# Performance work log

Measured on AMD Instinct MI355X. Metric: run time of the kernel, lower is better.

## Reference

```python
import jax, jax.numpy as jnp
import numpy as np
from jax import lax

B, T, D_IN = 16, 512, 128
H_ENC, D_LAT, H_CTX, H_PRED = 512, 256, 512, 512
K_STEPS, TEMP = 12, 0.1


def setup_inputs() -> dict:
    ks = jax.random.split(jax.random.key(0), 8)
    def w(i, fi, fo):
        return jax.random.normal(ks[i], (fi, fo), jnp.float32) * (1.0 / float(np.sqrt(fi)))
    return {
        "x": jax.random.normal(ks[0], (B, T, D_IN), jnp.float32),
        "enc_w1": w(1, D_IN, H_ENC), "enc_b1": jnp.zeros((H_ENC,), jnp.float32),
        "enc_w2": w(2, H_ENC, H_ENC), "enc_b2": jnp.zeros((H_ENC,), jnp.float32),
        "enc_w3": w(3, H_ENC, D_LAT), "enc_b3": jnp.zeros((D_LAT,), jnp.float32),
        "gru_wi": w(4, D_LAT, 3 * H_CTX), "gru_bi": jnp.zeros((3 * H_CTX,), jnp.float32),
        "gru_wh": w(5, H_CTX, 3 * H_CTX), "gru_bhn": jnp.zeros((H_CTX,), jnp.float32),
        "pred_w1": w(6, H_CTX, H_PRED), "pred_b1": jnp.zeros((H_PRED,), jnp.float32),
        "pred_w2": w(7, H_PRED, D_LAT), "pred_b2": jnp.zeros((D_LAT,), jnp.float32),
    }


def _gru(z, gru_wi, gru_bi, gru_wh, gru_bhn):
    # flax GRUCell: r=sig(Wir x + bir + Whr h); u=sig(Wiz x + biz + Whz h);
    Bsz = z.shape[0]
    H = gru_wh.shape[0]
    xi = z @ gru_wi + gru_bi          # [B, T, 3H] precomputed input projections
    xi = jnp.swapaxes(xi, 0, 1)       # [T, B, 3H]

    def step(h, x_t):
        hp = h @ gru_wh               # [B, 3H]
        xr, xu, xn = jnp.split(x_t, 3, axis=-1)
        hr, hu, hn = jnp.split(hp, 3, axis=-1)
        r = jax.nn.sigmoid(xr + hr)
        u = jax.nn.sigmoid(xu + hu)
        n = jnp.tanh(xn + r * (hn + gru_bhn))
        h_new = (1.0 - u) * n + u * h
        return h_new, h_new

    h0 = jnp.zeros((Bsz, H), z.dtype)
    _, outs = lax.scan(step, h0, xi)  # [T, B, H]
    return jnp.swapaxes(outs, 0, 1)   # [B, T, H]


def reference(x, enc_w1, enc_b1, enc_w2, enc_b2, enc_w3, enc_b3,
              gru_wi, gru_bi, gru_wh, gru_bhn,
              pred_w1, pred_b1, pred_w2, pred_b2):
    # Encoder MLP
    h = jax.nn.relu(x @ enc_w1 + enc_b1)
    h = jax.nn.relu(h @ enc_w2 + enc_b2)
    z = h @ enc_w3 + enc_b3                         # [B, T, D_LAT]
    # GRU context network
    c = _gru(z, gru_wi, gru_bi, gru_wh, gru_bhn)    # [B, T, H_CTX]
    # InfoNCE loss (prediction net is identical across k, so hoist it)
    c_t = c[:, :-K_STEPS, :].reshape(-1, c.shape[-1])   # [N, H_CTX], N=B*(T-K)
    p = jax.nn.relu(c_t @ pred_w1 + pred_b1) @ pred_w2 + pred_b2
    p = p / jnp.linalg.norm(p, axis=1, keepdims=True)   # [N, D_LAT]
    total = jnp.zeros((), z.dtype)
    for k in range(1, K_STEPS + 1):
        zt = z[:, k:T - K_STEPS + k, :].reshape(-1, z.shape[-1])
        zt = zt / jnp.linalg.norm(zt, axis=1, keepdims=True)
        sim = (p @ zt.T) / TEMP                         # [N, N]
        # -mean(diag(log_softmax)) = -mean(diag(sim) - logsumexp(sim, axis=1))
        total = total + (-jnp.mean(jnp.diagonal(sim) - jax.nn.logsumexp(sim, axis=1)))
    loss = total / K_STEPS
    return z, c, loss
```

## Files before the change

kernel.cpp:

```cpp
#include <hip/hip_runtime.h>
#include <cstdint>
#include <cstddef>

typedef unsigned short u16;
typedef unsigned int   u32;
typedef unsigned long long u64;
typedef __attribute__((ext_vector_type(8))) short bf16x8;
typedef __attribute__((ext_vector_type(4))) float f32x4;
typedef __attribute__((ext_vector_type(4))) unsigned int u32x4;

typedef __attribute__((address_space(1))) const unsigned int as1c_uint;
typedef __attribute__((address_space(3))) unsigned int as3_uint;

__device__ __forceinline__ void async16(const void* g, void* l) {
  __builtin_amdgcn_global_load_lds((as1c_uint*)g, (as3_uint*)l, 16, 0, 0);
}
__device__ __forceinline__ float bf2f(u16 u) {
  return __uint_as_float(((u32)u) << 16);
}
__device__ __forceinline__ u16 f2bf(float x) {
  u32 u = __float_as_uint(x);
  u32 r = u + 0x7FFFu + ((u >> 16) & 1u);
  return (u16)(r >> 16);
}

__device__ __forceinline__ u32 ld_u32_ic(const void* p) {
  u32 v;
  asm volatile("global_load_dword %0, %1, off sc0 sc1\n\ts_waitcnt vmcnt(0)"
               : "=v"(v) : "v"(p) : "memory");
  return v;
}
__device__ __forceinline__ void st_u32_ic(void* p, u32 v) {
  asm volatile("global_store_dword %0, %1, off sc0 sc1" :: "v"(p), "v"(v) : "memory");
}
__device__ __forceinline__ void ld_h64_ic(const void* p, u32x4& a, u32x4& b,
                                          u32x4& c, u32x4& d) {
  asm volatile(
      "global_load_dwordx4 %0, %4, off sc0 sc1\n\t"
      "global_load_dwordx4 %1, %4, off offset:16 sc0 sc1\n\t"
      "global_load_dwordx4 %2, %4, off offset:32 sc0 sc1\n\t"
      "global_load_dwordx4 %3, %4, off offset:48 sc0 sc1\n\t"
      "s_waitcnt vmcnt(0)"
      : "=&v"(a), "=&v"(b), "=&v"(c), "=&v"(d) : "v"(p) : "memory");
}

__global__ void cvt_k(const float4* __restrict__ in, ushort4* __restrict__ out) {
  int i = blockIdx.x * 256 + threadIdx.x;
  float4 v = in[i];
  ushort4 o;
  o.x = f2bf(v.x); o.y = f2bf(v.y); o.z = f2bf(v.z); o.w = f2bf(v.w);
  out[i] = o;
}

__global__ void tr_k(const float* __restrict__ in, u16* __restrict__ out, int K, int N) {
  __shared__ u16 t[32][33];
  int bn = blockIdx.x * 32, bk = blockIdx.y * 32;
  int x = threadIdx.x, y = threadIdx.y;
#pragma unroll
  for (int i = 0; i < 32; i += 8)
    t[y + i][x] = f2bf(in[(size_t)(bk + y + i) * N + bn + x]);
  __syncthreads();
#pragma unroll
  for (int i = 0; i < 32; i += 8)
    out[(size_t)(bn + y + i) * K + bk + x] = t[x][y + i];
}

__global__ __launch_bounds__(256) void gemm_k(
    const u16* __restrict__ A, const u16* __restrict__ Bt,
    const float* __restrict__ bias, u16* __restrict__ Cbf, float* __restrict__ Cf,
    int N, int K, int act) {
  __shared__ __align__(16) u16 As[128 * 32];
  __shared__ __align__(16) u16 Bs[128 * 32];
  int tid = threadIdx.x;
  int lane = tid & 63, w = tid >> 6;
  int wm = w >> 1, wn = w & 1;
  int mm = lane & 15, kh = lane >> 4;
  int m0 = blockIdx.y * 128, n0 = blockIdx.x * 128;

  f32x4 zero = {0.f, 0.f, 0.f, 0.f};
  f32x4 acc[4][4];
#pragma unroll
  for (int i = 0; i < 4; ++i)
#pragma unroll
    for (int j = 0; j < 4; ++j) acc[i][j] = zero;

  for (int kt = 0; kt < K; kt += 32) {
#pragma unroll
    for (int it = 0; it < 2; ++it) {
      int q = tid + it * 256;
      int row = q >> 2, kc = (q & 3) * 8;
      async16(A  + (size_t)(m0 + row) * K + kt + kc, &As[q * 8]);
      async16(Bt + (size_t)(n0 + row) * K + kt + kc, &Bs[q * 8]);
    }
    __syncthreads();
    bf16x8 av[4], bv[4];
#pragma unroll
    for (int i = 0; i < 4; ++i) {
      av[i] = *(const bf16x8*)&As[(wm * 64 + i * 16 + mm) * 32 + kh * 8];
      bv[i] = *(const bf16x8*)&Bs[(wn * 64 + i * 16 + mm) * 32 + kh * 8];
    }
#pragma unroll
    for (int im = 0; im < 4; ++im)
#pragma unroll
      for (int in = 0; in < 4; ++in)
        acc[im][in] = __builtin_amdgcn_mfma_f32_16x16x32_bf16(av[im], bv[in], acc[im][in], 0, 0, 0);
    __syncthreads();
  }

#pragma unroll
  for (int im = 0; im < 4; ++im)
#pragma unroll
    for (int in = 0; in < 4; ++in)
#pragma unroll
      for (int r = 0; r < 4; ++r) {
        int gm = m0 + wm * 64 + im * 16 + kh * 4 + r;
        int gn = n0 + wn * 64 + in * 16 + mm;
        float v = acc[im][in][r] + bias[gn];
        if (act) v = fmaxf(v, 0.f);
        size_t off = (size_t)gm * N + gn;
        if (Cbf) Cbf[off] = f2bf(v);
        if (Cf)  Cf[off]  = v;
      }
}

__global__ __launch_bounds__(256) void norm_k(const u16* __restrict__ in,
                                              u16* __restrict__ out, int pack) {
  int row = blockIdx.x * 4 + (threadIdx.x >> 6);
  int lane = threadIdx.x & 63;
  ushort4 v = ((const ushort4*)(in + (size_t)row * 256))[lane];
  float a = bf2f(v.x), b = bf2f(v.y), c = bf2f(v.z), d = bf2f(v.w);
  float s = a * a + b * b + c * c + d * d;
#pragma unroll
  for (int o = 32; o; o >>= 1) s += __shfl_xor(s, o);
  float rn = rsqrtf(s);
  int orow = row;
  if (pack) {
    int bb = row >> 9, tt = row & 511;
    if (tt >= 500) return;
    orow = bb * 500 + tt;
  }
  ushort4 o4;
  o4.x = f2bf(a * rn); o4.y = f2bf(b * rn);
  o4.z = f2bf(c * rn); o4.w = f2bf(d * rn);
  *(ushort4*)(out + (size_t)orow * 256 + lane * 4) = o4;
}

#define HS 520

__global__ __launch_bounds__(512, 1) void gru_k(
    const u16* __restrict__ xi, const float* __restrict__ WH,
    const float* __restrict__ BHN, float* __restrict__ cf,
    u16* __restrict__ cbf, u16* hbuf, u32* flags) {
  __shared__ __align__(16) u16 hs[16 * HS];
  __shared__ float xis[2 * 1536];
  __shared__ float gts[1536];
  __shared__ float hnf[512];

  int tid = threadIdx.x;
  int role = blockIdx.x;
  int c0 = role * 32;

  int lane = tid & 63, w = tid >> 6;
  int mm = lane & 15, kh = lane >> 4;

  bf16x8 wf[16];
  if (w < 6) {
    int gcol = (w >> 1) * 512 + c0 + (w & 1) * 16 + mm;
    int kb = kh * 8;
#pragma unroll
    for (int kk = 0; kk < 16; ++kk) {
      bf16x8 tf;
#pragma unroll
      for (int j = 0; j < 8; ++j)
        tf[j] = (short)f2bf(WH[(size_t)(kk * 32 + kb + j) * 1536 + gcol]);
      wf[kk] = tf;
    }
  }
  int cr = tid >> 4, cj = (tid & 15) * 2;
  float bhn0 = 0.f, bhn1 = 0.f;
  if (w < 4) { bhn0 = BHN[c0 + cj]; bhn1 = BHN[c0 + cj + 1]; }

  int tt = tid - 384;
  size_t xoff[12];
  u16 xpre[12];
  if (w >= 6) {
#pragma unroll
    for (int j = 0; j < 12; ++j) {
      int v = j * 128 + tt;
      int b = v / 96, q = v - b * 96;
      int gcol = (q >> 5) * 512 + c0 + (q & 31);
      xoff[j] = (size_t)b * 512 * 1536 + gcol;
      xis[v] = bf2f(xi[xoff[j]]);
    }
#pragma unroll
    for (int j = 0; j < 12; ++j) xpre[j] = xi[xoff[j] + 1536];
  }

  for (int t = 0; t < 512; ++t) {
    if (w < 4) {
      if (t == 0) {
        for (int i = tid; i < 16 * HS; i += 256) hs[i] = 0;
      } else {
        int iter = 0;
        const u32* fl = &flags[tid & 15];
        while (ld_u32_ic(fl) < (u32)t) { if (++iter > (1 << 22)) break; }
        const u16* hb = hbuf + (size_t)(t & 1) * 8192 + (tid >> 4) * 512 + (tid & 15) * 32;
        u32x4 a, b, c, d;
        ld_h64_ic(hb, a, b, c, d);
        u32x4* dst = (u32x4*)&hs[(tid >> 4) * HS + (tid & 15) * 32];
        dst[0] = a; dst[1] = b; dst[2] = c; dst[3] = d;
      }
    } else if (w >= 6) {
      if (t > 0) {
        int v = tt * 4;
        int b = v >> 5, col = v & 31;
        size_t co = ((size_t)b * 512 + (t - 1)) * 512 + c0 + col;
        float4 o;
        o.x = hnf[v]; o.y = hnf[v + 1]; o.z = hnf[v + 2]; o.w = hnf[v + 3];
        *(float4*)&cf[co] = o;
        uint2 pk;
        pk.x = (u32)f2bf(o.x) | ((u32)f2bf(o.y) << 16);
        pk.y = (u32)f2bf(o.z) | ((u32)f2bf(o.w) << 16);
        *(uint2*)&cbf[co] = pk;
      }
      if (t < 511) {
        float* xd = &xis[((t + 1) & 1) * 1536];
#pragma unroll
        for (int j = 0; j < 12; ++j) xd[j * 128 + tt] = bf2f(xpre[j]);
      }
      if (t < 510) {
        const u16* xs = xi + (size_t)(t + 2) * 1536;
#pragma unroll
        for (int j = 0; j < 12; ++j) xpre[j] = xs[xoff[j]];
      }
    }
    __syncthreads();

    if (w < 6) {
      f32x4 acc = {0.f, 0.f, 0.f, 0.f};
#pragma unroll
      for (int kk = 0; kk < 16; ++kk) {
        bf16x8 a = *(const bf16x8*)&hs[mm * HS + kk * 32 + kh * 8];
        acc = __builtin_amdgcn_mfma_f32_16x16x32_bf16(a, wf[kk], acc, 0, 0, 0);
      }
      int gc = (w >> 1) * 32 + (w & 1) * 16 + mm;
#pragma unroll
      for (int r = 0; r < 4; ++r) gts[(kh * 4 + r) * 96 + gc] = acc[r];
    }
    __syncthreads();

    if (w < 4) {
      const float* xc = &xis[(t & 1) * 1536] + cr * 96;
      const float* gr_ = &gts[cr * 96];
      float hp0 = bf2f(hs[cr * HS + c0 + cj]);
      float hp1 = bf2f(hs[cr * HS + c0 + cj + 1]);
      float r0 = 1.f / (1.f + __expf(-(xc[cj] + gr_[cj])));
      float u0 = 1.f / (1.f + __expf(-(xc[32 + cj] + gr_[32 + cj])));
      float nx0 = xc[64 + cj] + r0 * (gr_[64 + cj] + bhn0);
      float n0 = 1.f - 2.f / (__expf(2.f * nx0) + 1.f);
      float h0 = (1.f - u0) * n0 + u0 * hp0;
      float r1 = 1.f / (1.f + __expf(-(xc[cj + 1] + gr_[cj + 1])));
      float u1 = 1.f / (1.f + __expf(-(xc[33 + cj] + gr_[33 + cj])));
      float nx1 = xc[65 + cj] + r1 * (gr_[65 + cj] + bhn1);
      float n1 = 1.f - 2.f / (__expf(2.f * nx1) + 1.f);
      float h1v = (1.f - u1) * n1 + u1 * hp1;
      hnf[cr * 32 + cj] = h0;
      hnf[cr * 32 + cj + 1] = h1v;
      u32 pk = (u32)f2bf(h0) | ((u32)f2bf(h1v) << 16);
      st_u32_ic(hbuf + (size_t)((t + 1) & 1) * 8192 + cr * 512 + c0 + cj, pk);
      asm volatile("s_waitcnt vmcnt(0)" ::: "memory");
    }
    __syncthreads();
    if (tid == 0) st_u32_ic(&flags[role], (u32)(t + 1));
  }

  if (w >= 6) {
    int v = tt * 4;
    int b = v >> 5, col = v & 31;
    size_t co = ((size_t)b * 512 + 511) * 512 + c0 + col;
    float4 o;
    o.x = hnf[v]; o.y = hnf[v + 1]; o.z = hnf[v + 2]; o.w = hnf[v + 3];
    *(float4*)&cf[co] = o;
    uint2 pk;
    pk.x = (u32)f2bf(o.x) | ((u32)f2bf(o.y) << 16);
    pk.y = (u32)f2bf(o.z) | ((u32)f2bf(o.w) << 16);
    *(uint2*)&cbf[co] = pk;
  }
}

__global__ __launch_bounds__(256) void sgemm_k(
    const u16* __restrict__ P, const u16* __restrict__ Z,
    float* __restrict__ g, float* __restrict__ diag) {
  __shared__ __align__(16) u16 Ap[128 * 256];
  __shared__ __align__(16) u16 Bs[128 * 32];
  __shared__ float gacc[128 * 128];
  int tid = threadIdx.x;
  int lane = tid & 63, w = tid >> 6;
  int wm = w >> 1, wn = w & 1;
  int mm = lane & 15, kh = lane >> 4;
  int r0 = blockIdx.y * 128, t0 = blockIdx.x * 128;

#pragma unroll
  for (int it = 0; it < 16; ++it) {
    int q = tid + it * 256;
    int row = q >> 5, kc = (q & 31) * 8;
    async16(P + (size_t)(r0 + row) * 256 + kc, &Ap[q * 8]);
  }
  for (int i = tid; i < 128 * 128; i += 256) gacc[i] = 0.f;
  __syncthreads();

  f32x4 zero = {0.f, 0.f, 0.f, 0.f};
  for (int b = 0; b < 16; ++b) {
    int n0 = b * 512 + t0;
    f32x4 acc[4][4];
#pragma unroll
    for (int i = 0; i < 4; ++i)
#pragma unroll
      for (int j = 0; j < 4; ++j) acc[i][j] = zero;

    for (int kk = 0; kk < 8; ++kk) {
#pragma unroll
      for (int it = 0; it < 2; ++it) {
        int q = tid + it * 256;
        int row = q >> 2, kc = (q & 3) * 8;
        async16(Z + (size_t)(n0 + row) * 256 + kk * 32 + kc, &Bs[q * 8]);
      }
      __syncthreads();
      bf16x8 av[4], bv[4];
#pragma unroll
      for (int i = 0; i < 4; ++i) {
        av[i] = *(const bf16x8*)&Ap[(wm * 64 + i * 16 + mm) * 256 + kk * 32 + kh * 8];
        bv[i] = *(const bf16x8*)&Bs[(wn * 64 + i * 16 + mm) * 32 + kh * 8];
      }
#pragma unroll
      for (int im = 0; im < 4; ++im)
#pragma unroll
        for (int in = 0; in < 4; ++in)
          acc[im][in] = __builtin_amdgcn_mfma_f32_16x16x32_bf16(av[im], bv[in], acc[im][in], 0, 0, 0);
      __syncthreads();
    }
#pragma unroll
    for (int im = 0; im < 4; ++im)
#pragma unroll
      for (int in = 0; in < 4; ++in)
#pragma unroll
        for (int r = 0; r < 4; ++r) {
          int row = wm * 64 + im * 16 + kh * 4 + r;
          int col = wn * 64 + in * 16 + mm;
          float s10 = acc[im][in][r] * 10.f;
          gacc[row * 128 + col] += __expf(s10 - 10.f);
          int ig = r0 + row;
          if (ig < 8000) {
            int bi = ig / 500;
            if (bi == b) {
              int ti = ig - bi * 500;
              int dt = t0 + col - ti;
              if (dt >= 1 && dt <= 12) diag[(size_t)ig * 12 + dt - 1] = s10;
            }
          }
        }
  }
  __syncthreads();
  for (int i = tid; i < 128 * 128; i += 256) {
    int row = i >> 7, col = i & 127;
    g[(size_t)(r0 + row) * 512 + t0 + col] = gacc[i];
  }
}

__global__ __launch_bounds__(256) void win_k(const float* __restrict__ g,
                                             const float* __restrict__ diag,
                                             float* __restrict__ acc) {
  __shared__ float lo[4][16], hi[4][16];
  int w = threadIdx.x >> 6, lane = threadIdx.x & 63;
  int row = blockIdx.x * 4 + w;
  const float* gr = g + (size_t)row * 512;
  float4 a = ((const float4*)gr)[lane * 2];
  float4 b = ((const float4*)gr)[lane * 2 + 1];
  float s = a.x + a.y + a.z + a.w + b.x + b.y + b.z + b.w;
#pragma unroll
  for (int o = 32; o; o >>= 1) s += __shfl_xor(s, o);
  if (lane == 0) { lo[w][0]=a.x; lo[w][1]=a.y; lo[w][2]=a.z; lo[w][3]=a.w;
                   lo[w][4]=b.x; lo[w][5]=b.y; lo[w][6]=b.z; lo[w][7]=b.w; }
  if (lane == 1) { lo[w][8]=a.x; lo[w][9]=a.y; lo[w][10]=a.z; lo[w][11]=a.w; }
  if (lane == 62){ hi[w][0]=b.x; hi[w][1]=b.y; hi[w][2]=b.z; hi[w][3]=b.w; }
  if (lane == 63){ hi[w][4]=a.x; hi[w][5]=a.y; hi[w][6]=a.z; hi[w][7]=a.w;
                   hi[w][8]=b.x; hi[w][9]=b.y; hi[w][10]=b.z; hi[w][11]=b.w; }
  __syncthreads();
  float term = 0.f;
  if (lane < 12) {
    int k = lane + 1;
    float pre = 0.f, suf = 0.f;
#pragma unroll
    for (int j = 0; j < 12; ++j) {
      if (j < k) pre += lo[w][j];
      if (j >= k) suf += hi[w][j];
    }
    float W = s - pre - suf;
    term = diag[(size_t)row * 12 + lane] - __logf(W) - 10.f;
  }
#pragma unroll
  for (int o = 32; o; o >>= 1) term += __shfl_xor(term, o);
  if (lane == 0) atomicAdd(acc, term);
}

__global__ void fin_k(const float* acc, float* lout) {
  lout[0] = -acc[0] * (1.f / 96000.f);
}

extern "C" void kernel_launch(void* const* d_in, const int* in_sizes, int n_in,
                              void* d_out, int out_size, void* d_ws, size_t ws_size,
                              hipStream_t stream) {
  (void)in_sizes; (void)n_in; (void)out_size; (void)ws_size;
  const float* x    = (const float*)d_in[0];
  const float* ew1  = (const float*)d_in[1];
  const float* eb1  = (const float*)d_in[2];
  const float* ew2  = (const float*)d_in[3];
  const float* eb2  = (const float*)d_in[4];
  const float* ew3  = (const float*)d_in[5];
  const float* eb3  = (const float*)d_in[6];
  const float* gwi  = (const float*)d_in[7];
  const float* gbi  = (const float*)d_in[8];
  const float* gwh  = (const float*)d_in[9];
  const float* gbhn = (const float*)d_in[10];
  const float* pw1  = (const float*)d_in[11];
  const float* pb1  = (const float*)d_in[12];
  const float* pw2  = (const float*)d_in[13];
  const float* pb2  = (const float*)d_in[14];

  char* W = (char*)d_ws;
  u32*   flags = (u32*)(W + 64);
  float* lacc = (float*)(W + 2048);
  u16*   w1T  = (u16*)(W + 4096);
  u16*   w2T  = (u16*)(W + 135168);
  u16*   w3T  = (u16*)(W + 659456);
  u16*   wiT  = (u16*)(W + 921600);
  u16*   p1T  = (u16*)(W + 1708032);
  u16*   p2T  = (u16*)(W + 2232320);
  u16*   hbuf = (u16*)(W + 2494464);
  float* diag = (float*)(W + 2527232);
  u16*   zhat = (u16*)(W + 2911232);
  u16*   zbf  = (u16*)(W + 7105536);
  u16*   cbf  = (u16*)(W + 7105536);
  u16*   ppk  = (u16*)(W + 7105536);
  u16*   xi   = (u16*)(W + 15494144);
  u16*   xbf  = (u16*)(W + 15494144);
  u16*   h1   = (u16*)(W + 17591296);
  u16*   h2   = (u16*)(W + 25979904);
  float* g    = (float*)(W + 15494144);

  float* zf    = (float*)d_out;
  float* cf    = zf + 2097152;
  float* lout  = zf + 6291456;

  hipMemsetAsync(d_ws, 0, 4096, stream);

  cvt_k<<<1024, 256, 0, stream>>>((const float4*)x, (ushort4*)xbf);

  dim3 tb(32, 8);
  tr_k<<<dim3(16, 4),  tb, 0, stream>>>(ew1, w1T, 128, 512);
  tr_k<<<dim3(16, 16), tb, 0, stream>>>(ew2, w2T, 512, 512);
  tr_k<<<dim3(8, 16),  tb, 0, stream>>>(ew3, w3T, 512, 256);
  tr_k<<<dim3(48, 8),  tb, 0, stream>>>(gwi, wiT, 256, 1536);
  tr_k<<<dim3(16, 16), tb, 0, stream>>>(pw1, p1T, 512, 512);
  tr_k<<<dim3(8, 16),  tb, 0, stream>>>(pw2, p2T, 512, 256);

  gemm_k<<<dim3(4, 64),  256, 0, stream>>>(xbf,  w1T, eb1, h1,  nullptr, 512, 128, 1);
  gemm_k<<<dim3(4, 64),  256, 0, stream>>>(h1,   w2T, eb2, h2,  nullptr, 512, 512, 1);
  gemm_k<<<dim3(2, 64),  256, 0, stream>>>(h2,   w3T, eb3, zbf, zf,      256, 512, 0);
  norm_k<<<2048, 256, 0, stream>>>(zbf, zhat, 0);
  gemm_k<<<dim3(12, 64), 256, 0, stream>>>(zbf,  wiT, gbi, xi,  nullptr, 1536, 256, 0);
  gru_k<<<16, 512, 0, stream>>>(xi, gwh, gbhn, cf, cbf, hbuf, flags);
  gemm_k<<<dim3(4, 64),  256, 0, stream>>>(cbf,  p1T, pb1, h1,  nullptr, 512, 512, 1);
  gemm_k<<<dim3(2, 64),  256, 0, stream>>>(h1,   p2T, pb2, h2,  nullptr, 256, 512, 0);
  norm_k<<<2048, 256, 0, stream>>>(h2, ppk, 1);
  sgemm_k<<<dim3(4, 63), 256, 0, stream>>>(ppk, zhat, g, diag);
  win_k<<<2000, 256, 0, stream>>>(g, diag, lacc);
  fin_k<<<1, 1, 0, stream>>>(lacc, lout);
}
```

Baseline: 1.903 ms.

## Tag GRU hidden-state exchange with step counters instead of separate flags

Replaces the per-block flag-based handshake in the persistent GRU kernel with hidden-state words that carry the timestep tag alongside the data. Readers spin on the data itself until all tags match, which removes the separate flag poll, the store fence, and the post-barrier flag write from each of the 512 sequential steps. In exchange the exchange buffer doubles in size, each reader loads twice the bytes per poll, and correctness relies on 64-bit stores being seen atomically. Workspace offsets are shifted to fit the larger buffer.

```diff
diff --git a/kernel.cpp b/kernel.cpp
--- a/kernel.cpp
+++ b/kernel.cpp
@@ -24,24 +24,23 @@
   return (u16)(r >> 16);
 }
 
-__device__ __forceinline__ u32 ld_u32_ic(const void* p) {
-  u32 v;
-  asm volatile("global_load_dword %0, %1, off sc0 sc1\n\ts_waitcnt vmcnt(0)"
-               : "=v"(v) : "v"(p) : "memory");
-  return v;
-}
-__device__ __forceinline__ void st_u32_ic(void* p, u32 v) {
-  asm volatile("global_store_dword %0, %1, off sc0 sc1" :: "v"(p), "v"(v) : "memory");
-}
-__device__ __forceinline__ void ld_h64_ic(const void* p, u32x4& a, u32x4& b,
-                                          u32x4& c, u32x4& d) {
+__device__ __forceinline__ void st_u64_ic(void* p, u64 v) {
+  asm volatile("global_store_dwordx2 %0, %1, off sc0 sc1" :: "v"(p), "v"(v) : "memory");
+}
+__device__ __forceinline__ void ld8_ic(const void* p, u32x4* r) {
   asm volatile(
-      "global_load_dwordx4 %0, %4, off sc0 sc1\n\t"
-      "global_load_dwordx4 %1, %4, off offset:16 sc0 sc1\n\t"
-      "global_load_dwordx4 %2, %4, off offset:32 sc0 sc1\n\t"
-      "global_load_dwordx4 %3, %4, off offset:48 sc0 sc1\n\t"
+      "global_load_dwordx4 %0, %8, off sc0 sc1\n\t"
+      "global_load_dwordx4 %1, %8, off offset:16 sc0 sc1\n\t"
+      "global_load_dwordx4 %2, %8, off offset:32 sc0 sc1\n\t"
+      "global_load_dwordx4 %3, %8, off offset:48 sc0 sc1\n\t"
+      "global_load_dwordx4 %4, %8, off offset:64 sc0 sc1\n\t"
+      "global_load_dwordx4 %5, %8, off offset:80 sc0 sc1\n\t"
+      "global_load_dwordx4 %6, %8, off offset:96 sc0 sc1\n\t"
+      "global_load_dwordx4 %7, %8, off offset:112 sc0 sc1\n\t"
       "s_waitcnt vmcnt(0)"
-      : "=&v"(a), "=&v"(b), "=&v"(c), "=&v"(d) : "v"(p) : "memory");
+      : "=&v"(r[0]), "=&v"(r[1]), "=&v"(r[2]), "=&v"(r[3]),
+        "=&v"(r[4]), "=&v"(r[5]), "=&v"(r[6]), "=&v"(r[7])
+      : "v"(p) : "memory");
 }
 
 __global__ void cvt_k(const float4* __restrict__ in, ushort4* __restrict__ out) {
@@ -150,7 +149,7 @@
 __global__ __launch_bounds__(512, 1) void gru_k(
     const u16* __restrict__ xi, const float* __restrict__ WH,
     const float* __restrict__ BHN, float* __restrict__ cf,
-    u16* __restrict__ cbf, u16* hbuf, u32* flags) {
+    u16* __restrict__ cbf, u64* hbuf2) {
   __shared__ __align__(16) u16 hs[16 * HS];
   __shared__ float xis[2 * 1536];
   __shared__ float gts[1536];
@@ -201,14 +200,20 @@
       if (t == 0) {
         for (int i = tid; i < 16 * HS; i += 256) hs[i] = 0;
       } else {
+        const u64* hb = hbuf2 + (size_t)(t & 1) * 4096 + (tid >> 4) * 256 + (tid & 15) * 16;
+        u32x4 r[8];
+        u32 tv = (u32)t;
         int iter = 0;
-        const u32* fl = &flags[tid & 15];
-        while (ld_u32_ic(fl) < (u32)t) { if (++iter > (1 << 22)) break; }
-        const u16* hb = hbuf + (size_t)(t & 1) * 8192 + (tid >> 4) * 512 + (tid & 15) * 32;
-        u32x4 a, b, c, d;
-        ld_h64_ic(hb, a, b, c, d);
-        u32x4* dst = (u32x4*)&hs[(tid >> 4) * HS + (tid & 15) * 32];
-        dst[0] = a; dst[1] = b; dst[2] = c; dst[3] = d;
+        for (;;) {
+          ld8_ic(hb, r);
+          u32 bad = 0;
+#pragma unroll
+          for (int k = 0; k < 8; ++k) bad |= (r[k][1] ^ tv) | (r[k][3] ^ tv);
+          if (!bad || ++iter > (1 << 20)) break;
+        }
+        u32* dst = (u32*)&hs[(tid >> 4) * HS + (tid & 15) * 32];
+#pragma unroll
+        for (int k = 0; k < 8; ++k) { dst[2 * k] = r[k][0]; dst[2 * k + 1] = r[k][2]; }
       }
     } else if (w >= 6) {
       if (t > 0) {
@@ -266,12 +271,11 @@
       float h1v = (1.f - u1) * n1 + u1 * hp1;
       hnf[cr * 32 + cj] = h0;
       hnf[cr * 32 + cj + 1] = h1v;
-      u32 pk = (u32)f2bf(h0) | ((u32)f2bf(h1v) << 16);
-      st_u32_ic(hbuf + (size_t)((t + 1) & 1) * 8192 + cr * 512 + c0 + cj, pk);
-      asm volatile("s_waitcnt vmcnt(0)" ::: "memory");
+      u64 pk = ((u64)(u32)(t + 1) << 32) |
+               (u64)(((u32)f2bf(h1v) << 16) | (u32)f2bf(h0));
+      st_u64_ic(hbuf2 + (size_t)((t + 1) & 1) * 4096 + cr * 256 + ((c0 + cj) >> 1), pk);
     }
     __syncthreads();
-    if (tid == 0) st_u32_ic(&flags[role], (u32)(t + 1));
   }
 
   if (w >= 6) {
@@ -428,25 +432,24 @@
   const float* pb2  = (const float*)d_in[14];
 
   char* W = (char*)d_ws;
-  u32*   flags = (u32*)(W + 64);
-  float* lacc = (float*)(W + 2048);
-  u16*   w1T  = (u16*)(W + 4096);
-  u16*   w2T  = (u16*)(W + 135168);
-  u16*   w3T  = (u16*)(W + 659456);
-  u16*   wiT  = (u16*)(W + 921600);
-  u16*   p1T  = (u16*)(W + 1708032);
-  u16*   p2T  = (u16*)(W + 2232320);
-  u16*   hbuf = (u16*)(W + 2494464);
-  float* diag = (float*)(W + 2527232);
-  u16*   zhat = (u16*)(W + 2911232);
-  u16*   zbf  = (u16*)(W + 7105536);
-  u16*   cbf  = (u16*)(W + 7105536);
-  u16*   ppk  = (u16*)(W + 7105536);
-  u16*   xi   = (u16*)(W + 15494144);
-  u16*   xbf  = (u16*)(W + 15494144);
-  u16*   h1   = (u16*)(W + 17591296);
-  u16*   h2   = (u16*)(W + 25979904);
-  float* g    = (float*)(W + 15494144);
+  float* lacc  = (float*)(W + 2048);
+  u16*   w1T   = (u16*)(W + 4096);
+  u16*   w2T   = (u16*)(W + 135168);
+  u16*   w3T   = (u16*)(W + 659456);
+  u16*   wiT   = (u16*)(W + 921600);
+  u16*   p1T   = (u16*)(W + 1708032);
+  u16*   p2T   = (u16*)(W + 2232320);
+  u64*   hbuf2 = (u64*)(W + 2494464);
+  float* diag  = (float*)(W + 2560000);
+  u16*   zhat  = (u16*)(W + 2944000);
+  u16*   zbf   = (u16*)(W + 7138304);
+  u16*   cbf   = (u16*)(W + 7138304);
+  u16*   ppk   = (u16*)(W + 7138304);
+  u16*   xi    = (u16*)(W + 15526912);
+  u16*   xbf   = (u16*)(W + 15526912);
+  u16*   h1    = (u16*)(W + 17624064);
+  u16*   h2    = (u16*)(W + 26012672);
+  float* g     = (float*)(W + 15526912);
 
   float* zf    = (float*)d_out;
   float* cf    = zf + 2097152;
@@ -469,7 +472,7 @@
   gemm_k<<<dim3(2, 64),  256, 0, stream>>>(h2,   w3T, eb3, zbf, zf,      256, 512, 0);
   norm_k<<<2048, 256, 0, stream>>>(zbf, zhat, 0);
   gemm_k<<<dim3(12, 64), 256, 0, stream>>>(zbf,  wiT, gbi, xi,  nullptr, 1536, 256, 0);
-  gru_k<<<16, 512, 0, stream>>>(xi, gwh, gbhn, cf, cbf, hbuf, flags);
+  gru_k<<<16, 512, 0, stream>>>(xi, gwh, gbhn, cf, cbf, hbuf2);
   gemm_k<<<dim3(4, 64),  256, 0, stream>>>(cbf,  p1T, pb1, h1,  nullptr, 512, 512, 1);
   gemm_k<<<dim3(2, 64),  256, 0, stream>>>(h1,   p2T, pb2, h2,  nullptr, 256, 512, 0);
   norm_k<<<2048, 256, 0, stream>>>(h2, ppk, 1);
```

Result: slower. 2.001 ms (+5.1%).
